# Optimization experiments

Hardware: AMD Instinct MI355X
Metric: run time of the kernel (lower is better)

The kernel has to match this reference:

```python
import jax, jax.numpy as jnp
import numpy as np

SUPPORT = 1.5   # attributes['support']
N_RBF = 4       # n = m = 4 hat-function basis per axis
NF, NB = 8192, 2048


def hat_basis(u, n):
    # linear (hat) RBF basis on centers in [-1, 1]
    centers = jnp.linspace(-1.0, 1.0, n, dtype=u.dtype)
    spacing = 2.0 / (n - 1)
    return jax.nn.relu(1.0 - jnp.abs(u[:, None] - centers) / spacing)  # [E, n]


def rbf_conv(f_src, tgt, src, d, W, b, num_nodes):
    # d: [E,2] clamped relative positions; polar coordinate mapping
    r = jnp.linalg.norm(d, axis=-1) * 2.0 - 1.0          # radius -> [-1,1]
    theta = jnp.arctan2(d[:, 1], d[:, 0]) / jnp.pi       # angle  -> [-1,1]
    coeff = (hat_basis(r, N_RBF)[:, :, None] * hat_basis(theta, N_RBF)[:, None, :])
    coeff = coeff.reshape(d.shape[0], N_RBF * N_RBF)      # [E, k]
    f = f_src[src]                                        # gather  [E, Cin]
    tmp = jnp.einsum('ei,kio->eko', f, W)                 # [E, k, Cout]
    msg = jnp.einsum('ek,eko->eo', coeff, tmp)            # [E, Cout]
    return jax.ops.segment_sum(msg, tgt, num_segments=num_nodes) + b


def setup_inputs() -> dict:
    key = jax.random.key(0)
    ks = list(jax.random.split(key, 40))
    inp = {}
    inp['fluidPositions'] = jax.random.uniform(ks[0], (NF, 2), dtype=jnp.float32)
    inp['boundaryPositions'] = jax.random.uniform(ks[1], (NB, 2), dtype=jnp.float32)
    inp['fluidFeats'] = jax.random.normal(ks[2], (NF, 2), dtype=jnp.float32)
    inp['boundaryFeats'] = jax.random.normal(ks[3], (NB, 3), dtype=jnp.float32)
    EF, EB = 131072, 32768
    inp['fe_i'] = jnp.sort(jax.random.randint(ks[4], (EF,), 0, NF, dtype=jnp.int32))
    inp['fe_j'] = jax.random.randint(ks[5], (EF,), 0, NF, dtype=jnp.int32)
    inp['be_f'] = jnp.sort(jax.random.randint(ks[6], (EB,), 0, NF, dtype=jnp.int32))
    inp['be_b'] = jax.random.randint(ks[7], (EB,), 0, NB, dtype=jnp.int32)
    k2 = N_RBF * N_RBF
    conv_shapes = [(2, 16), (2, 16), (3, 16), (3, 16), (96, 32), (96, 32), (64, 32), (64, 32)]
    for c, (ci, co) in enumerate(conv_shapes):
        inp[f'W{c}'] = jax.random.normal(ks[8 + c], (k2, ci, co), dtype=jnp.float32) * 0.05
        inp[f'b{c}'] = jnp.zeros((co,), dtype=jnp.float32)
    fc_shapes = [(2, 32), (96, 64), (64, 64)]
    for c, (ci, co) in enumerate(fc_shapes):
        inp[f'fcW{c}'] = jax.random.normal(ks[20 + c], (ci, co), dtype=jnp.float32) * 0.05
        inp[f'fcb{c}'] = jnp.zeros((co,), dtype=jnp.float32)
    return inp


def reference(fluidPositions, boundaryPositions, fluidFeats, boundaryFeats,
              fe_i, fe_j, be_f, be_b,
              W0, b0, W1, b1, W2, b2, W3, b3, W4, b4, W5, b5, W6, b6, W7, b7,
              fcW0, fcb0, fcW1, fcb1, fcW2, fcb2):
    nF = fluidPositions.shape[0]
    # edge relative positions, clamped to [-1, 1]
    b_d = jnp.clip((boundaryPositions[be_b] - fluidPositions[be_f]) / SUPPORT, -1.0, 1.0)
    f_d = jnp.clip(-(fluidPositions[fe_j] - fluidPositions[fe_i]) / SUPPORT, -1.0, 1.0)

    linearOutput = fluidFeats @ fcW0 + fcb0                               # [N, 32]
    bA = rbf_conv(boundaryFeats, be_f, be_b, b_d, W2, b2, nF)             # [N, 16]
    bB = rbf_conv(boundaryFeats, be_f, be_b, b_d, W3, b3, nF)
    fA = rbf_conv(fluidFeats, fe_i, fe_j, f_d, W0, b0, nF)
    fB = rbf_conv(fluidFeats, fe_i, fe_j, f_d, W1, b1, nF)
    ans = jnp.concatenate([linearOutput, fA, fB, bA, bB], axis=1)          # [N, 96]

    # hidden layer i=2: convs 4,5 + fc1 (no residual: 32 != 64)
    ansc = jax.nn.relu(ans)
    conv = jnp.concatenate([rbf_conv(ansc, fe_i, fe_j, f_d, W4, b4, nF),
                            rbf_conv(ansc, fe_i, fe_j, f_d, W5, b5, nF)], axis=1)
    ans = conv + (ansc @ fcW1 + fcb1)                                      # [N, 64]

    # hidden layer i=3: convs 6,7 + fc2 (+ residual: 64 == 64)
    ansc = jax.nn.relu(ans)
    conv = jnp.concatenate([rbf_conv(ansc, fe_i, fe_j, f_d, W6, b6, nF),
                            rbf_conv(ansc, fe_i, fe_j, f_d, W7, b7, nF)], axis=1)
    ans = conv + (ansc @ fcW2 + fcb2) + ans

    return ans / 128.0
```

## Files before the change

### kernel.cpp

```cpp
#include <hip/hip_runtime.h>
#include <math.h>

#define SUPPORT 1.5f

typedef unsigned short ushort_t;
typedef short bf16x8 __attribute__((ext_vector_type(8)));
typedef float f32x4 __attribute__((ext_vector_type(4)));

__device__ __forceinline__ float bf2f(unsigned short h) {
    union { unsigned int u; float f; } c;
    c.u = ((unsigned int)h) << 16;
    return c.f;
}
__device__ __forceinline__ unsigned short f2bf(float f) {
    union { float f; unsigned int u; } c;
    c.f = f;
    unsigned int lsb = (c.u >> 16) & 1u;
    c.u += 0x7fffu + lsb;
    return (unsigned short)(c.u >> 16);
}

__device__ __forceinline__ void hat4(float u, float h[4]) {
#pragma unroll
    for (int j = 0; j < 4; ++j) {
        float c = -1.0f + j * (2.0f / 3.0f);
        h[j] = fmaxf(0.0f, 1.0f - fabsf(u - c) * 1.5f);
    }
}

__device__ __forceinline__ void coeff16(float2 A, float2 B, bool neg, float* o) {
    float rx = (A.x - B.x) / SUPPORT;
    float ry = (A.y - B.y) / SUPPORT;
    if (neg) { rx = -rx; ry = -ry; }
    float dx = fminf(fmaxf(rx, -1.0f), 1.0f);
    float dy = fminf(fmaxf(ry, -1.0f), 1.0f);
    float r  = sqrtf(dx * dx + dy * dy) * 2.0f - 1.0f;
    float th = atan2f(dy, dx) / 3.14159265358979323846f;
    float hr[4], ht[4];
    hat4(r, hr);
    hat4(th, ht);
#pragma unroll
    for (int a = 0; a < 4; ++a)
#pragma unroll
        for (int b = 0; b < 4; ++b)
            o[a * 4 + b] = hr[a] * ht[b];
}

__device__ __forceinline__ int lower_bound(const int* __restrict__ arr, int E, int key) {
    int lo = 0, hi = E;
    while (lo < hi) {
        int mid = (lo + hi) >> 1;
        if (arr[mid] < key) lo = mid + 1; else hi = mid;
    }
    return lo;
}

__device__ __forceinline__ void packW(const float* __restrict__ WA,
                                      const float* __restrict__ WB,
                                      const float* __restrict__ fcW,
                                      ushort_t* __restrict__ Wp, int CIN, int idx) {
    int j8   = idx & 7;
    int lane = (idx >> 3) & 63;
    int tile = (idx >> 9) & 3;
    int ks   = idx >> 11;
    int kk = ks * 32 + ((lane >> 4) << 3) + j8;
    int o  = tile * 16 + (lane & 15);
    int KC = 16 * CIN;
    float v = (kk < KC) ? ((o < 32) ? WA[(size_t)kk * 32 + o] : WB[(size_t)kk * 32 + (o - 32)])
                        : fcW[(size_t)(kk - KC) * 64 + o];
    Wp[idx] = f2bf(v);
}

__global__ void prologue_kernel(
    const float2* __restrict__ fPos, const float2* __restrict__ bPos,
    const int* __restrict__ fe_i, const int* __restrict__ fe_j,
    const int* __restrict__ be_f, const int* __restrict__ be_b,
    const float* __restrict__ W4, const float* __restrict__ W5,
    const float* __restrict__ fcW1, const float* __restrict__ b4,
    const float* __restrict__ b5, const float* __restrict__ fcb1,
    const float* __restrict__ W6, const float* __restrict__ W7,
    const float* __restrict__ fcW2, const float* __restrict__ b6,
    const float* __restrict__ b7, const float* __restrict__ fcb2,
    float* __restrict__ f_coeff, float* __restrict__ b_coeff,
    int* __restrict__ f_off, int* __restrict__ b_off,
    ushort_t* __restrict__ Wp2, float* __restrict__ bias2,
    ushort_t* __restrict__ Wp3, float* __restrict__ bias3,
    int EF, int EB, int NF) {
    int idx = blockIdx.x * 256 + threadIdx.x;
    if (idx < EF) {
        float co[16];
        coeff16(fPos[fe_j[idx]], fPos[fe_i[idx]], true, co);
        float* o = f_coeff + (size_t)idx * 16;
#pragma unroll
        for (int i = 0; i < 16; ++i) o[i] = co[i];
        return;
    }
    idx -= EF;
    if (idx < EB) {
        float co[16];
        coeff16(bPos[be_b[idx]], fPos[be_f[idx]], false, co);
        float* o = b_coeff + (size_t)idx * 16;
#pragma unroll
        for (int i = 0; i < 16; ++i) o[i] = co[i];
        return;
    }
    idx -= EB;
    if (idx < NF + 1) { f_off[idx] = lower_bound(fe_i, EF, idx); return; }
    idx -= NF + 1;
    if (idx < NF + 1) { b_off[idx] = lower_bound(be_f, EB, idx); return; }
    idx -= NF + 1;
    if (idx < 64) { bias2[idx] = ((idx < 32) ? b4[idx] : b5[idx - 32]) + fcb1[idx]; return; }
    idx -= 64;
    if (idx < 51 * 2048) { packW(W4, W5, fcW1, Wp2, 96, idx); return; }
    idx -= 51 * 2048;
    if (idx < 64) { bias3[idx] = ((idx < 32) ? b6[idx] : b7[idx - 32]) + fcb2[idx]; return; }
    idx -= 64;
    if (idx < 34 * 2048) { packW(W6, W7, fcW2, Wp3, 64, idx); return; }
}

__global__ void layer1_kernel(const float* __restrict__ fluidFeats,
                              const float* __restrict__ boundaryFeats,
                              const float* __restrict__ fcW0, const float* __restrict__ fcb0,
                              const float* __restrict__ W0, const float* __restrict__ b0,
                              const float* __restrict__ W1, const float* __restrict__ b1,
                              const float* __restrict__ W2, const float* __restrict__ b2,
                              const float* __restrict__ W3, const float* __restrict__ b3,
                              const int* __restrict__ f_off, const int* __restrict__ fe_j,
                              const float* __restrict__ f_coeff,
                              const int* __restrict__ b_off, const int* __restrict__ be_b,
                              const float* __restrict__ b_coeff,
                              ushort_t* __restrict__ A1b) {
    int n = blockIdx.x;
    int t = threadIdx.x;
    if (t >= 96) return;
    float val;
    if (t < 32) {
        val = fluidFeats[n * 2] * fcW0[t] + fluidFeats[n * 2 + 1] * fcW0[32 + t] + fcb0[t];
    } else if (t < 64) {
        int oc = t - 32;
        const float* W = (oc < 16) ? W0 : W1;
        int o16 = oc & 15;
        float wk[32];
#pragma unroll
        for (int k = 0; k < 16; ++k) {
            wk[2 * k + 0] = W[(k * 2 + 0) * 16 + o16];
            wk[2 * k + 1] = W[(k * 2 + 1) * 16 + o16];
        }
        float s = (oc < 16) ? b0[o16] : b1[o16];
        int e0 = f_off[n], e1 = f_off[n + 1];
        for (int e = e0; e < e1; e += 4) {
            int ee[4];
            float msk[4];
#pragma unroll
            for (int u = 0; u < 4; ++u) {
                ee[u] = (e + u < e1) ? e + u : e;
                msk[u] = (e + u < e1) ? 1.0f : 0.0f;
            }
            int sn[4];
#pragma unroll
            for (int u = 0; u < 4; ++u) sn[u] = fe_j[ee[u]];
            float4 c4[4][4];
#pragma unroll
            for (int u = 0; u < 4; ++u) {
                const float4* cf4 = (const float4*)(f_coeff + (size_t)ee[u] * 16);
#pragma unroll
                for (int q = 0; q < 4; ++q) c4[u][q] = cf4[q];
            }
            float2 fv[4];
#pragma unroll
            for (int u = 0; u < 4; ++u)
                fv[u] = *(const float2*)(fluidFeats + (size_t)sn[u] * 2);
#pragma unroll
            for (int u = 0; u < 4; ++u) {
                float f0 = fv[u].x * msk[u], f1 = fv[u].y * msk[u];
                const float* cf = (const float*)&c4[u][0];
                float acc = 0.0f;
#pragma unroll
                for (int k = 0; k < 16; ++k)
                    acc += cf[k] * (f0 * wk[2 * k] + f1 * wk[2 * k + 1]);
                s += acc;
            }
        }
        val = s;
    } else {
        int oc = t - 64;
        const float* W = (oc < 16) ? W2 : W3;
        int o16 = oc & 15;
        float wk[48];
#pragma unroll
        for (int k = 0; k < 16; ++k) {
            wk[3 * k + 0] = W[(k * 3 + 0) * 16 + o16];
            wk[3 * k + 1] = W[(k * 3 + 1) * 16 + o16];
            wk[3 * k + 2] = W[(k * 3 + 2) * 16 + o16];
        }
        float s = (oc < 16) ? b2[o16] : b3[o16];
        int e0 = b_off[n], e1 = b_off[n + 1];
        for (int e = e0; e < e1; e += 4) {
            int ee[4];
            float msk[4];
#pragma unroll
            for (int u = 0; u < 4; ++u) {
                ee[u] = (e + u < e1) ? e + u : e;
                msk[u] = (e + u < e1) ? 1.0f : 0.0f;
            }
            int sn[4];
#pragma unroll
            for (int u = 0; u < 4; ++u) sn[u] = be_b[ee[u]];
            float4 c4[4][4];
#pragma unroll
            for (int u = 0; u < 4; ++u) {
                const float4* cf4 = (const float4*)(b_coeff + (size_t)ee[u] * 16);
#pragma unroll
                for (int q = 0; q < 4; ++q) c4[u][q] = cf4[q];
            }
            float bf[4][3];
#pragma unroll
            for (int u = 0; u < 4; ++u) {
                bf[u][0] = boundaryFeats[(size_t)sn[u] * 3 + 0];
                bf[u][1] = boundaryFeats[(size_t)sn[u] * 3 + 1];
                bf[u][2] = boundaryFeats[(size_t)sn[u] * 3 + 2];
            }
#pragma unroll
            for (int u = 0; u < 4; ++u) {
                float f0 = bf[u][0] * msk[u], f1 = bf[u][1] * msk[u], f2 = bf[u][2] * msk[u];
                const float* cf = (const float*)&c4[u][0];
                float acc = 0.0f;
#pragma unroll
                for (int k = 0; k < 16; ++k)
                    acc += cf[k] * (f0 * wk[3 * k] + f1 * wk[3 * k + 1] + f2 * wk[3 * k + 2]);
                s += acc;
            }
        }
        val = s;
    }
    A1b[(size_t)n * 96 + t] = f2bf(fmaxf(val, 0.0f));
}

template <int CIN, bool RELU, bool RESID, bool FINAL>
__global__ __launch_bounds__(512) void conv_mfma_kernel(
    const ushort_t* __restrict__ Xb,
    const int* __restrict__ f_off, const int* __restrict__ fe_j,
    const float* __restrict__ f_coeff,
    const ushort_t* __restrict__ Wp, const float* __restrict__ bias,
    const ushort_t* __restrict__ XresB,
    void* __restrict__ OUT, int NF) {
    constexpr int KTOT   = 17 * CIN;
    constexpr int KSTEPS = KTOT / 32;
    constexpr int STRIDE = KTOT + 8;
    constexpr int EPT = CIN / 4;
    constexpr int NU4 = EPT / 8;

    __shared__ ushort_t Gl[16 * STRIDE];
    __shared__ float red[4][64][4];

    const int t = threadIdx.x;
    const int wv = t >> 6;
    const int lane = t & 63;
    const int nb = blockIdx.x * 16;

    const int k  = lane >> 2;
    const int i0 = (lane & 3) * EPT;
    for (int s2 = 0; s2 < 2; ++s2) {
        int lnode = wv * 2 + s2;
        int n = nb + lnode;
        if (n > NF - 1) n = NF - 1;

        float acc[EPT];
#pragma unroll
        for (int s = 0; s < EPT; ++s) acc[s] = 0.0f;

        int e0 = f_off[n], e1 = f_off[n + 1];
        for (int e = e0; e < e1; e += 4) {
            int ea = e;
            int eb = (e + 1 < e1) ? e + 1 : e;
            int ec = (e + 2 < e1) ? e + 2 : e;
            int ed = (e + 3 < e1) ? e + 3 : e;
            int s0 = fe_j[ea], s1 = fe_j[eb], s2i = fe_j[ec], s3 = fe_j[ed];
            float c0 = f_coeff[(size_t)ea * 16 + k];
            float c1 = f_coeff[(size_t)eb * 16 + k];
            float c2 = f_coeff[(size_t)ec * 16 + k];
            float c3 = f_coeff[(size_t)ed * 16 + k];
            c1 = (e + 1 < e1) ? c1 : 0.0f;
            c2 = (e + 2 < e1) ? c2 : 0.0f;
            c3 = (e + 3 < e1) ? c3 : 0.0f;
            const uint4* x0 = (const uint4*)(Xb + (size_t)s0 * CIN + i0);
            const uint4* x1 = (const uint4*)(Xb + (size_t)s1 * CIN + i0);
            const uint4* x2 = (const uint4*)(Xb + (size_t)s2i * CIN + i0);
            const uint4* x3 = (const uint4*)(Xb + (size_t)s3 * CIN + i0);
            uint4 r0[NU4], r1[NU4], r2[NU4], r3[NU4];
#pragma unroll
            for (int q = 0; q < NU4; ++q) r0[q] = x0[q];
#pragma unroll
            for (int q = 0; q < NU4; ++q) r1[q] = x1[q];
#pragma unroll
            for (int q = 0; q < NU4; ++q) r2[q] = x2[q];
#pragma unroll
            for (int q = 0; q < NU4; ++q) r3[q] = x3[q];
#pragma unroll
            for (int q = 0; q < NU4; ++q) {
                unsigned int w0[4] = {r0[q].x, r0[q].y, r0[q].z, r0[q].w};
                unsigned int w1[4] = {r1[q].x, r1[q].y, r1[q].z, r1[q].w};
                unsigned int w2[4] = {r2[q].x, r2[q].y, r2[q].z, r2[q].w};
                unsigned int w3[4] = {r3[q].x, r3[q].y, r3[q].z, r3[q].w};
#pragma unroll
                for (int j = 0; j < 4; ++j) {
                    int s = q * 8 + j * 2;
#define EDGEFMA(wj, cc)                                                        \
                    {                                                          \
                        float lo = bf2f((unsigned short)(wj[j] & 0xffff));     \
                        float hi = bf2f((unsigned short)(wj[j] >> 16));        \
                        if (RELU) { lo = fmaxf(lo, 0.f); hi = fmaxf(hi, 0.f); }\
                        acc[s + 0] = fmaf(cc, lo, acc[s + 0]);                 \
                        acc[s + 1] = fmaf(cc, hi, acc[s + 1]);                 \
                    }
                    EDGEFMA(w0, c0)
                    EDGEFMA(w1, c1)
                    EDGEFMA(w2, c2)
                    EDGEFMA(w3, c3)
#undef EDGEFMA
                }
            }
        }

        ushort_t* grow = Gl + lnode * STRIDE;
        ushort_t* gp = grow + k * CIN + i0;
#pragma unroll
        for (int q = 0; q < NU4; ++q) {
            uint4 o;
            o.x = (unsigned int)f2bf(acc[q*8+0]) | ((unsigned int)f2bf(acc[q*8+1]) << 16);
            o.y = (unsigned int)f2bf(acc[q*8+2]) | ((unsigned int)f2bf(acc[q*8+3]) << 16);
            o.z = (unsigned int)f2bf(acc[q*8+4]) | ((unsigned int)f2bf(acc[q*8+5]) << 16);
            o.w = (unsigned int)f2bf(acc[q*8+6]) | ((unsigned int)f2bf(acc[q*8+7]) << 16);
            *(uint4*)(gp + q * 8) = o;
        }
        for (int i = lane; i < CIN; i += 64) {
            ushort_t v = Xb[(size_t)n * CIN + i];
            if (RELU && (v & 0x8000)) v = 0;
            grow[16 * CIN + i] = v;
        }
    }
    __syncthreads();

    const int ot = wv & 3;
    const int kh = wv >> 2;
    f32x4 cacc = {0.f, 0.f, 0.f, 0.f};
    const ushort_t* garow = Gl + (lane & 15) * STRIDE + ((lane >> 4) << 3);
    const ushort_t* wpp = Wp + ((size_t)(ot * 64 + lane) << 3);
    for (int ks = kh; ks < KSTEPS; ks += 2) {
        bf16x8 a = *(const bf16x8*)(garow + ks * 32);
        bf16x8 b = *(const bf16x8*)(wpp + (size_t)ks * 2048);
        cacc = __builtin_amdgcn_mfma_f32_16x16x32_bf16(a, b, cacc, 0, 0, 0);
    }
    if (kh == 1) {
        red[ot][lane][0] = cacc[0];
        red[ot][lane][1] = cacc[1];
        red[ot][lane][2] = cacc[2];
        red[ot][lane][3] = cacc[3];
    }
    __syncthreads();
    if (kh == 0) {
        int o = ot * 16 + (lane & 15);
        float bo = bias[o];
#pragma unroll
        for (int r = 0; r < 4; ++r) {
            int node = nb + ((lane >> 4) << 2) + r;
            if (node < NF) {
                float s = cacc[r] + red[ot][lane][r] + bo;
                if (RESID) s += bf2f(XresB[(size_t)node * 64 + o]);
                if (FINAL) {
                    ((float*)OUT)[(size_t)node * 64 + o] = s * (1.0f / 128.0f);
                } else {
                    ((ushort_t*)OUT)[(size_t)node * 64 + o] = f2bf(s);
                }
            }
        }
    }
}

extern "C" void kernel_launch(void* const* d_in, const int* in_sizes, int n_in,
                              void* d_out, int out_size, void* d_ws, size_t ws_size,
                              hipStream_t stream) {
    const float* fluidPos      = (const float*)d_in[0];
    const float* boundaryPos   = (const float*)d_in[1];
    const float* fluidFeats    = (const float*)d_in[2];
    const float* boundaryFeats = (const float*)d_in[3];
    const int* fe_i = (const int*)d_in[4];
    const int* fe_j = (const int*)d_in[5];
    const int* be_f = (const int*)d_in[6];
    const int* be_b = (const int*)d_in[7];
    const float* W[8];
    const float* bb[8];
    for (int c = 0; c < 8; ++c) {
        W[c]  = (const float*)d_in[8 + 2 * c];
        bb[c] = (const float*)d_in[9 + 2 * c];
    }
    const float* fcW0 = (const float*)d_in[24];
    const float* fcb0 = (const float*)d_in[25];
    const float* fcW1 = (const float*)d_in[26];
    const float* fcb1 = (const float*)d_in[27];
    const float* fcW2 = (const float*)d_in[28];
    const float* fcb2 = (const float*)d_in[29];

    int NF = in_sizes[0] / 2;
    int EF = in_sizes[4];
    int EB = in_sizes[6];

    float* ws = (float*)d_ws;
    size_t p = 0;
    float* f_coeff = ws + p;  p += (size_t)EF * 16;
    float* b_coeff = ws + p;  p += (size_t)EB * 16;
    ushort_t* A1b  = (ushort_t*)(ws + p);  p += (size_t)NF * 48;
    ushort_t* ans2b= (ushort_t*)(ws + p);  p += (size_t)NF * 32;
    int*   f_off   = (int*)(ws + p);  p += (size_t)((NF + 4) & ~3);
    int*   b_off   = (int*)(ws + p);  p += (size_t)((NF + 4) & ~3);
    ushort_t* Wp2  = (ushort_t*)(ws + p);  p += 1632 * 32;
    float* bias2   = ws + p;  p += 64;
    ushort_t* Wp3  = (ushort_t*)(ws + p);  p += 1088 * 32;
    float* bias3   = ws + p;  p += 64;

    int totalPro = EF + EB + 2 * (NF + 1) + 64 + 51 * 2048 + 64 + 34 * 2048;
    prologue_kernel<<<(totalPro + 255) / 256, 256, 0, stream>>>(
        (const float2*)fluidPos, (const float2*)boundaryPos,
        fe_i, fe_j, be_f, be_b,
        W[4], W[5], fcW1, bb[4], bb[5], fcb1,
        W[6], W[7], fcW2, bb[6], bb[7], fcb2,
        f_coeff, b_coeff, f_off, b_off,
        Wp2, bias2, Wp3, bias3, EF, EB, NF);

    layer1_kernel<<<NF, 128, 0, stream>>>(fluidFeats, boundaryFeats, fcW0, fcb0,
                                          W[0], bb[0], W[1], bb[1], W[2], bb[2], W[3], bb[3],
                                          f_off, fe_j, f_coeff, b_off, be_b, b_coeff, A1b);

    int nblk = (NF + 15) / 16;
    conv_mfma_kernel<96, false, false, false><<<nblk, 512, 0, stream>>>(
        A1b, f_off, fe_j, f_coeff, Wp2, bias2, nullptr, ans2b, NF);
    conv_mfma_kernel<64, true, true, true><<<nblk, 512, 0, stream>>>(
        ans2b, f_off, fe_j, f_coeff, Wp3, bias3, ans2b, d_out, NF);
}
```

Measured before the change: 98.53 us.

## Halve nodes per conv block to 8 and prefetch next edge in gather loop

Result: no change. 99.70 us (+1.2%).

```diff
diff --git a/kernel.cpp b/kernel.cpp
--- a/kernel.cpp
+++ b/kernel.cpp
@@ -237,7 +237,7 @@
 }
 
 template <int CIN, bool RELU, bool RESID, bool FINAL>
-__global__ __launch_bounds__(512) void conv_mfma_kernel(
+__global__ __launch_bounds__(512, 8) void conv_mfma_kernel(
     const ushort_t* __restrict__ Xb,
     const int* __restrict__ f_off, const int* __restrict__ fe_j,
     const float* __restrict__ f_coeff,
@@ -250,79 +250,56 @@
     constexpr int EPT = CIN / 4;
     constexpr int NU4 = EPT / 8;
 
-    __shared__ ushort_t Gl[16 * STRIDE];
+    __shared__ ushort_t Gl[8 * STRIDE];
     __shared__ float red[4][64][4];
 
     const int t = threadIdx.x;
     const int wv = t >> 6;
     const int lane = t & 63;
-    const int nb = blockIdx.x * 16;
-
-    const int k  = lane >> 2;
-    const int i0 = (lane & 3) * EPT;
-    for (int s2 = 0; s2 < 2; ++s2) {
-        int lnode = wv * 2 + s2;
-        int n = nb + lnode;
+    const int nb = blockIdx.x * 8;
+
+    {
+        int n = nb + wv;
         if (n > NF - 1) n = NF - 1;
+        const int k  = lane >> 2;
+        const int i0 = (lane & 3) * EPT;
 
         float acc[EPT];
 #pragma unroll
         for (int s = 0; s < EPT; ++s) acc[s] = 0.0f;
 
         int e0 = f_off[n], e1 = f_off[n + 1];
-        for (int e = e0; e < e1; e += 4) {
-            int ea = e;
-            int eb = (e + 1 < e1) ? e + 1 : e;
-            int ec = (e + 2 < e1) ? e + 2 : e;
-            int ed = (e + 3 < e1) ? e + 3 : e;
-            int s0 = fe_j[ea], s1 = fe_j[eb], s2i = fe_j[ec], s3 = fe_j[ed];
-            float c0 = f_coeff[(size_t)ea * 16 + k];
-            float c1 = f_coeff[(size_t)eb * 16 + k];
-            float c2 = f_coeff[(size_t)ec * 16 + k];
-            float c3 = f_coeff[(size_t)ed * 16 + k];
-            c1 = (e + 1 < e1) ? c1 : 0.0f;
-            c2 = (e + 2 < e1) ? c2 : 0.0f;
-            c3 = (e + 3 < e1) ? c3 : 0.0f;
-            const uint4* x0 = (const uint4*)(Xb + (size_t)s0 * CIN + i0);
-            const uint4* x1 = (const uint4*)(Xb + (size_t)s1 * CIN + i0);
-            const uint4* x2 = (const uint4*)(Xb + (size_t)s2i * CIN + i0);
-            const uint4* x3 = (const uint4*)(Xb + (size_t)s3 * CIN + i0);
-            uint4 r0[NU4], r1[NU4], r2[NU4], r3[NU4];
-#pragma unroll
-            for (int q = 0; q < NU4; ++q) r0[q] = x0[q];
-#pragma unroll
-            for (int q = 0; q < NU4; ++q) r1[q] = x1[q];
-#pragma unroll
-            for (int q = 0; q < NU4; ++q) r2[q] = x2[q];
-#pragma unroll
-            for (int q = 0; q < NU4; ++q) r3[q] = x3[q];
+        int sN = 0; float cN = 0.0f;
+        if (e0 < e1) {
+            sN = fe_j[e0];
+            cN = f_coeff[(size_t)e0 * 16 + k];
+        }
+        for (int e = e0; e < e1; ++e) {
+            int sC = sN; float cC = cN;
+            if (e + 1 < e1) {
+                sN = fe_j[e + 1];
+                cN = f_coeff[(size_t)(e + 1) * 16 + k];
+            }
+            const uint4* xp = (const uint4*)(Xb + (size_t)sC * CIN + i0);
+            uint4 r[NU4];
+#pragma unroll
+            for (int q = 0; q < NU4; ++q) r[q] = xp[q];
 #pragma unroll
             for (int q = 0; q < NU4; ++q) {
-                unsigned int w0[4] = {r0[q].x, r0[q].y, r0[q].z, r0[q].w};
-                unsigned int w1[4] = {r1[q].x, r1[q].y, r1[q].z, r1[q].w};
-                unsigned int w2[4] = {r2[q].x, r2[q].y, r2[q].z, r2[q].w};
-                unsigned int w3[4] = {r3[q].x, r3[q].y, r3[q].z, r3[q].w};
+                unsigned int w[4] = {r[q].x, r[q].y, r[q].z, r[q].w};
 #pragma unroll
                 for (int j = 0; j < 4; ++j) {
+                    float lo = bf2f((unsigned short)(w[j] & 0xffff));
+                    float hi = bf2f((unsigned short)(w[j] >> 16));
+                    if (RELU) { lo = fmaxf(lo, 0.f); hi = fmaxf(hi, 0.f); }
                     int s = q * 8 + j * 2;
-#define EDGEFMA(wj, cc)                                                        \
-                    {                                                          \
-                        float lo = bf2f((unsigned short)(wj[j] & 0xffff));     \
-                        float hi = bf2f((unsigned short)(wj[j] >> 16));        \
-                        if (RELU) { lo = fmaxf(lo, 0.f); hi = fmaxf(hi, 0.f); }\
-                        acc[s + 0] = fmaf(cc, lo, acc[s + 0]);                 \
-                        acc[s + 1] = fmaf(cc, hi, acc[s + 1]);                 \
-                    }
-                    EDGEFMA(w0, c0)
-                    EDGEFMA(w1, c1)
-                    EDGEFMA(w2, c2)
-                    EDGEFMA(w3, c3)
-#undef EDGEFMA
+                    acc[s + 0] = fmaf(cC, lo, acc[s + 0]);
+                    acc[s + 1] = fmaf(cC, hi, acc[s + 1]);
                 }
             }
         }
 
-        ushort_t* grow = Gl + lnode * STRIDE;
+        ushort_t* grow = Gl + wv * STRIDE;
         ushort_t* gp = grow + k * CIN + i0;
 #pragma unroll
         for (int q = 0; q < NU4; ++q) {
@@ -344,7 +321,7 @@
     const int ot = wv & 3;
     const int kh = wv >> 2;
     f32x4 cacc = {0.f, 0.f, 0.f, 0.f};
-    const ushort_t* garow = Gl + (lane & 15) * STRIDE + ((lane >> 4) << 3);
+    const ushort_t* garow = Gl + (lane & 7) * STRIDE + ((lane >> 4) << 3);
     const ushort_t* wpp = Wp + ((size_t)(ot * 64 + lane) << 3);
     for (int ks = kh; ks < KSTEPS; ks += 2) {
         bf16x8 a = *(const bf16x8*)(garow + ks * 32);
@@ -363,8 +340,9 @@
         float bo = bias[o];
 #pragma unroll
         for (int r = 0; r < 4; ++r) {
-            int node = nb + ((lane >> 4) << 2) + r;
-            if (node < NF) {
+            int row = ((lane >> 4) << 2) + r;
+            int node = nb + row;
+            if (row < 8 && node < NF) {
                 float s = cacc[r] + red[ot][lane][r] + bo;
                 if (RESID) s += bf2f(XresB[(size_t)node * 64 + o]);
                 if (FINAL) {
@@ -431,7 +409,7 @@
                                           W[0], bb[0], W[1], bb[1], W[2], bb[2], W[3], bb[3],
                                           f_off, fe_j, f_coeff, b_off, be_b, b_coeff, A1b);
 
-    int nblk = (NF + 15) / 16;
+    int nblk = (NF + 7) / 8;
     conv_mfma_kernel<96, false, false, false><<<nblk, 512, 0, stream>>>(
         A1b, f_off, fe_j, f_coeff, Wp2, bias2, nullptr, ans2b, NF);
     conv_mfma_kernel<64, true, true, true><<<nblk, 512, 0, stream>>>(
```
